# Kernel optimization log

Measured on AMD Instinct MI355X. Metric: run time of the kernel, lower is better.

## Reference

```python
import jax, jax.numpy as jnp
import numpy as np

B, C, H, W = 16, 128, 64, 64
C_OUT = 256
N_BANDS = 4
KS = [3, 5, 7, 11]
BN_EPS = 1e-5


def setup_inputs() -> dict:
    key = jax.random.key(0)
    ks = jax.random.split(key, 16)
    inp = {
        'x': jax.random.normal(ks[0], (B, C, H, W), dtype=jnp.float32),
        'conv_w0': jax.random.normal(ks[1], (C, 1, 3), dtype=jnp.float32) * 0.2,
        'conv_w1': jax.random.normal(ks[2], (C, 1, 5), dtype=jnp.float32) * 0.2,
        'conv_w2': jax.random.normal(ks[3], (C, 1, 7), dtype=jnp.float32) * 0.2,
        'conv_w3': jax.random.normal(ks[4], (C, 1, 11), dtype=jnp.float32) * 0.2,
        'bn_gamma': jax.random.uniform(ks[5], (N_BANDS, C), dtype=jnp.float32, minval=0.5, maxval=1.5),
        'bn_beta': jax.random.normal(ks[6], (N_BANDS, C), dtype=jnp.float32) * 0.1,
        'bn_mean': jax.random.normal(ks[7], (N_BANDS, C), dtype=jnp.float32) * 0.1,
        'bn_var': jax.random.uniform(ks[8], (N_BANDS, C), dtype=jnp.float32, minval=0.5, maxval=1.5),
        'scale_weights': jnp.ones((N_BANDS,), dtype=jnp.float32),
        'alpha': jnp.float32(0.5),
        'proj_w': jax.random.normal(ks[9], (C_OUT, C * N_BANDS), dtype=jnp.float32) * 0.04,
        'proj_b': jax.random.normal(ks[10], (C_OUT,), dtype=jnp.float32) * 0.02,
    }
    return inp


def _dwconv1d(xc, w):
    # xc: [B, C, L], w: [C, 1, k] depthwise, 'same' padding for odd k
    k = w.shape[-1]
    return jax.lax.conv_general_dilated(
        xc, w, window_strides=(1,), padding=[(k // 2, k // 2)],
        feature_group_count=xc.shape[1], dimension_numbers=('NCH', 'OIH', 'NCH'))


def _forward(x, conv_w0, conv_w1, conv_w2, conv_w3, bn_gamma, bn_beta, bn_mean,
             bn_var, scale_weights, alpha, proj_w, proj_b):
    b, c, h, w = x.shape
    L = h * w
    xs = x.reshape(b, c, L)                      # [B, C, L] (== x.view.transpose.transpose)
    norm_w = jax.nn.softmax(scale_weights)       # [n_bands]

    # --- multi-scale depthwise conv branch: conv -> BN(eval) -> GELU -> scale ---
    conv_bands = []
    for i, cw in enumerate([conv_w0, conv_w1, conv_w2, conv_w3]):
        y = _dwconv1d(xs, cw)                    # [B, C, L]
        inv = jax.lax.rsqrt(bn_var[i] + BN_EPS)  # [C]
        y = (y - bn_mean[i][:, None]) * (inv * bn_gamma[i])[:, None] + bn_beta[i][:, None]
        y = jax.nn.gelu(y, approximate=False)    # exact erf GELU (torch default)
        conv_bands.append(y.transpose(0, 2, 1) * norm_w[i])  # [B, L, C]

    # --- frequency band branch (interpolate to size L is identity: conv keeps L) ---
    xt = xs.transpose(0, 2, 1)                   # [B, L, C]
    Xf = jnp.fft.rfft(xt, axis=1)                # [B, n_freqs, C]
    n_freqs = L // 2 + 1
    band_size = n_freqs // N_BANDS
    fidx = jnp.arange(n_freqs)
    alpha_s = jax.nn.sigmoid(alpha)
    fused = []
    for i in range(N_BANDS):
        start = i * band_size
        end = (i + 1) * band_size if i < N_BANDS - 1 else n_freqs
        mask = (fidx >= start) & (fidx < end)
        band = jnp.fft.irfft(jnp.where(mask[None, :, None], Xf, 0), n=L, axis=1)
        fused.append(alpha_s * conv_bands[i] + (1.0 - alpha_s) * band)

    cat = jnp.concatenate(fused, axis=-1)        # [B, L, n_bands*C]
    out = cat @ proj_w.T + proj_b                # [B, L, C_out]
    return out.transpose(0, 2, 1).reshape(b, -1, h, w)


def reference(x, conv_w0, conv_w1, conv_w2, conv_w3, bn_gamma, bn_beta, bn_mean,
              bn_var, scale_weights, alpha, proj_w, proj_b):
    return _forward(x, conv_w0, conv_w1, conv_w2, conv_w3, bn_gamma, bn_beta,
                    bn_mean, bn_var, scale_weights, alpha, proj_w, proj_b)
```

## Files before the change

### kernel.cpp

```cpp
#include <hip/hip_runtime.h>
#include <math.h>

constexpr int LEN = 4096;
constexpr int NTHREADS = 512;
constexpr int PELEM = LEN / NTHREADS;
constexpr float INVN = 1.0f / 4096.0f;
constexpr float RHALF = 0.70710678118654752440f;

typedef __attribute__((ext_vector_type(8))) short bf16x8;
typedef __attribute__((ext_vector_type(4))) float f32x4;

#define APHYS(I) ((I) + ((I) >> 5))
#define TPHYS(I) ((I) + ((I) >> 5))
#define ZOFF 8

__device__ __forceinline__ unsigned short f2bf(float f) {
    unsigned u = __float_as_uint(f);
    unsigned r = (u + 0x7fffu + ((u >> 16) & 1u)) >> 16;
    return (unsigned short)r;
}

__device__ __forceinline__ int digitrev8(int j) {
    return ((j & 7) << 9) | (((j >> 3) & 7) << 6) | (((j >> 6) & 7) << 3) | (j >> 9);
}

__device__ __forceinline__ void cmul(float ar, float ai, float br, float bi,
                                     float& cr, float& ci) {
    cr = ar * br - ai * bi;
    ci = ar * bi + ai * br;
}

__device__ void dif_fft8(float* __restrict__ ar, float* __restrict__ ai,
                         const float* __restrict__ twr, const float* __restrict__ twi,
                         int tid) {
#pragma unroll
    for (int s = 0; s < 4; ++s) {
        __syncthreads();
        const int eshift = 3 * (3 - s);
        const int E = 1 << eshift;
        int j = tid & (E - 1);
        int g = tid >> eshift;
        int base = (g << (eshift + 3)) + j;

        float xr[8], xi[8];
#pragma unroll
        for (int m = 0; m < 8; ++m) {
            int idx = APHYS(base + (m << eshift));
            xr[m] = ar[idx]; xi[m] = ai[idx];
        }
        float b0r = xr[0] + xr[4], b0i = xi[0] + xi[4];
        float b1r = xr[1] + xr[5], b1i = xi[1] + xi[5];
        float b2r = xr[2] + xr[6], b2i = xi[2] + xi[6];
        float b3r = xr[3] + xr[7], b3i = xi[3] + xi[7];
        float c0r = xr[0] - xr[4], c0i = xi[0] - xi[4];
        float c1r = xr[1] - xr[5], c1i = xi[1] - xi[5];
        float c2r = xr[2] - xr[6], c2i = xi[2] - xi[6];
        float c3r = xr[3] - xr[7], c3i = xi[3] - xi[7];
        float d1r = RHALF * (c1r + c1i), d1i = RHALF * (c1i - c1r);
        float d2r = c2i,               d2i = -c2r;
        float d3r = -RHALF * (c3r - c3i), d3i = -RHALF * (c3r + c3i);
        float t0r = b0r + b2r, t0i = b0i + b2i;
        float t1r = b0r - b2r, t1i = b0i - b2i;
        float t2r = b1r + b3r, t2i = b1i + b3i;
        float t3r = b1r - b3r, t3i = b1i - b3i;
        xr[0] = t0r + t2r; xi[0] = t0i + t2i;
        xr[2] = t1r + t3i; xi[2] = t1i - t3r;
        xr[4] = t0r - t2r; xi[4] = t0i - t2i;
        xr[6] = t1r - t3i; xi[6] = t1i + t3r;
        t0r = c0r + d2r; t0i = c0i + d2i;
        t1r = c0r - d2r; t1i = c0i - d2i;
        t2r = d1r + d3r; t2i = d1i + d3i;
        t3r = d1r - d3r; t3i = d1i - d3i;
        xr[1] = t0r + t2r; xi[1] = t0i + t2i;
        xr[3] = t1r + t3i; xi[3] = t1i - t3r;
        xr[5] = t0r - t2r; xi[5] = t0i - t2i;
        xr[7] = t1r - t3i; xi[7] = t1i + t3r;

        if (s < 3) {
            int k1 = j << (3 * s);
            float w1r = twr[TPHYS(k1)], w1i = twi[TPHYS(k1)];
            float w2r, w2i, w3r, w3i, w4r, w4i, w5r, w5i, w6r, w6i, w7r, w7i;
            cmul(w1r, w1i, w1r, w1i, w2r, w2i);
            cmul(w2r, w2i, w1r, w1i, w3r, w3i);
            cmul(w2r, w2i, w2r, w2i, w4r, w4i);
            cmul(w4r, w4i, w1r, w1i, w5r, w5i);
            cmul(w4r, w4i, w2r, w2i, w6r, w6i);
            cmul(w4r, w4i, w3r, w3i, w7r, w7i);
            float orr, oii;
            cmul(xr[1], xi[1], w1r, w1i, orr, oii); xr[1] = orr; xi[1] = oii;
            cmul(xr[2], xi[2], w2r, w2i, orr, oii); xr[2] = orr; xi[2] = oii;
            cmul(xr[3], xi[3], w3r, w3i, orr, oii); xr[3] = orr; xi[3] = oii;
            cmul(xr[4], xi[4], w4r, w4i, orr, oii); xr[4] = orr; xi[4] = oii;
            cmul(xr[5], xi[5], w5r, w5i, orr, oii); xr[5] = orr; xi[5] = oii;
            cmul(xr[6], xi[6], w6r, w6i, orr, oii); xr[6] = orr; xi[6] = oii;
            cmul(xr[7], xi[7], w7r, w7i, orr, oii); xr[7] = orr; xi[7] = oii;
        }
#pragma unroll
        for (int m = 0; m < 8; ++m) {
            int idx = APHYS(base + (m << eshift));
            ar[idx] = xr[m]; ai[idx] = xi[m];
        }
    }
    __syncthreads();
}

__device__ void dit_ifft8(float* __restrict__ ar, float* __restrict__ ai,
                          const float* __restrict__ twr, const float* __restrict__ twi,
                          int tid) {
#pragma unroll
    for (int s = 0; s < 4; ++s) {
        __syncthreads();
        const int eshift = 3 * s;
        const int E = 1 << eshift;
        int j = tid & (E - 1);
        int g = tid >> eshift;
        int base = (g << (eshift + 3)) + j;

        float xr[8], xi[8];
#pragma unroll
        for (int m = 0; m < 8; ++m) {
            int idx = APHYS(base + (m << eshift));
            xr[m] = ar[idx]; xi[m] = ai[idx];
        }
        if (s > 0) {
            int k1 = j << (3 * (3 - s));
            float w1r = twr[TPHYS(k1)], w1i = -twi[TPHYS(k1)];
            float w2r, w2i, w3r, w3i, w4r, w4i, w5r, w5i, w6r, w6i, w7r, w7i;
            cmul(w1r, w1i, w1r, w1i, w2r, w2i);
            cmul(w2r, w2i, w1r, w1i, w3r, w3i);
            cmul(w2r, w2i, w2r, w2i, w4r, w4i);
            cmul(w4r, w4i, w1r, w1i, w5r, w5i);
            cmul(w4r, w4i, w2r, w2i, w6r, w6i);
            cmul(w4r, w4i, w3r, w3i, w7r, w7i);
            float orr, oii;
            cmul(xr[1], xi[1], w1r, w1i, orr, oii); xr[1] = orr; xi[1] = oii;
            cmul(xr[2], xi[2], w2r, w2i, orr, oii); xr[2] = orr; xi[2] = oii;
            cmul(xr[3], xi[3], w3r, w3i, orr, oii); xr[3] = orr; xi[3] = oii;
            cmul(xr[4], xi[4], w4r, w4i, orr, oii); xr[4] = orr; xi[4] = oii;
            cmul(xr[5], xi[5], w5r, w5i, orr, oii); xr[5] = orr; xi[5] = oii;
            cmul(xr[6], xi[6], w6r, w6i, orr, oii); xr[6] = orr; xi[6] = oii;
            cmul(xr[7], xi[7], w7r, w7i, orr, oii); xr[7] = orr; xi[7] = oii;
        }
        float b0r = xr[0] + xr[4], b0i = xi[0] + xi[4];
        float b1r = xr[1] + xr[5], b1i = xi[1] + xi[5];
        float b2r = xr[2] + xr[6], b2i = xi[2] + xi[6];
        float b3r = xr[3] + xr[7], b3i = xi[3] + xi[7];
        float c0r = xr[0] - xr[4], c0i = xi[0] - xi[4];
        float c1r = xr[1] - xr[5], c1i = xi[1] - xi[5];
        float c2r = xr[2] - xr[6], c2i = xi[2] - xi[6];
        float c3r = xr[3] - xr[7], c3i = xi[3] - xi[7];
        float d1r = RHALF * (c1r - c1i), d1i = RHALF * (c1r + c1i);
        float d2r = -c2i,              d2i = c2r;
        float d3r = -RHALF * (c3r + c3i), d3i = RHALF * (c3r - c3i);
        float t0r = b0r + b2r, t0i = b0i + b2i;
        float t1r = b0r - b2r, t1i = b0i - b2i;
        float t2r = b1r + b3r, t2i = b1i + b3i;
        float t3r = b1r - b3r, t3i = b1i - b3i;
        xr[0] = t0r + t2r; xi[0] = t0i + t2i;
        xr[2] = t1r - t3i; xi[2] = t1i + t3r;
        xr[4] = t0r - t2r; xi[4] = t0i - t2i;
        xr[6] = t1r + t3i; xi[6] = t1i - t3r;
        t0r = c0r + d2r; t0i = c0i + d2i;
        t1r = c0r - d2r; t1i = c0i - d2i;
        t2r = d1r + d3r; t2i = d1i + d3i;
        t3r = d1r - d3r; t3i = d1i - d3i;
        xr[1] = t0r + t2r; xi[1] = t0i + t2i;
        xr[3] = t1r - t3i; xi[3] = t1i + t3r;
        xr[5] = t0r - t2r; xi[5] = t0i - t2i;
        xr[7] = t1r + t3i; xi[7] = t1i - t3r;

#pragma unroll
        for (int m = 0; m < 8; ++m) {
            int idx = APHYS(base + (m << eshift));
            ar[idx] = xr[m]; ai[idx] = xi[m];
        }
    }
    __syncthreads();
}

__global__ __launch_bounds__(512) void k_bands(
    const float* __restrict__ x,
    const float* __restrict__ cw0, const float* __restrict__ cw1,
    const float* __restrict__ cw2, const float* __restrict__ cw3,
    const float* __restrict__ bng, const float* __restrict__ bnb,
    const float* __restrict__ bnm, const float* __restrict__ bnv,
    const float* __restrict__ sw, const float* __restrict__ alp,
    unsigned int* __restrict__ Fu) {
    __shared__ float zr[LEN + 16], zi[LEN + 16];
    __shared__ float wr[4224], wi[4224];
    __shared__ float twr[528], twi[528];

    const int tid = threadIdx.x;
    const int pair = blockIdx.x;
    const int b = blockIdx.y;
    const int c0 = 2 * pair, c1 = c0 + 1;

    const float* xp0 = x + ((size_t)b * 128 + c0) * LEN;
    const float* xp1 = xp0 + LEN;
#pragma unroll
    for (int p = 0; p < PELEM; ++p) {
        int l = tid + NTHREADS * p;
        float a0 = xp0[l], a1 = xp1[l];
        zr[ZOFF + l] = a0; zi[ZOFF + l] = a1;
        wr[APHYS(l)] = a0; wi[APHYS(l)] = a1;
    }
    if (tid < 8) {
        zr[tid] = 0.f; zi[tid] = 0.f;
        zr[ZOFF + LEN + tid] = 0.f; zi[ZOFF + LEN + tid] = 0.f;
    }
    {
        int jj = tid;
        float ang = -(float)(2.0 * M_PI / 4096.0) * (float)jj;
        float sv, cv;
        sincosf(ang, &sv, &cv);
        twr[TPHYS(jj)] = cv; twi[TPHYS(jj)] = sv;
    }
    dif_fft8(wr, wi, twr, twi, tid);

    float Zre[PELEM], Zim[PELEM];
#pragma unroll
    for (int p = 0; p < PELEM; ++p) {
        int l = tid + NTHREADS * p;
        Zre[p] = wr[APHYS(l)]; Zim[p] = wi[APHYS(l)];
    }

    float s0w = sw[0], s1w = sw[1], s2w = sw[2], s3w = sw[3];
    float mx = fmaxf(fmaxf(s0w, s1w), fmaxf(s2w, s3w));
    float e0 = expf(s0w - mx), e1 = expf(s1w - mx), e2 = expf(s2w - mx), e3 = expf(s3w - mx);
    float esum = e0 + e1 + e2 + e3;
    float nwv[4] = {e0 / esum, e1 / esum, e2 / esum, e3 / esum};
    float alpha_s = 1.0f / (1.0f + expf(-alp[0]));
    float oma = 1.0f - alpha_s;

    const float* cwp[4] = {cw0, cw1, cw2, cw3};
    const int kk4[4] = {3, 5, 7, 11};

    float accr[PELEM], acci[PELEM];
#pragma unroll
    for (int p = 0; p < PELEM; ++p) { accr[p] = 0.f; acci[p] = 0.f; }

    unsigned int* dst = Fu + (size_t)b * (512 * LEN / 2);
    const int n = tid & 15;

#pragma unroll
    for (int band = 0; band < 4; ++band) {
        if (band < 3) {
            const int fs = band * 512, fe = fs + 512;
#pragma unroll
            for (int p = 0; p < PELEM; ++p) {
                int j = tid + NTHREADS * p;
                int f = digitrev8(j);
                int fi = (f <= 2048) ? f : (4096 - f);
                bool keep = (fi >= fs) && (fi < fe);
                wr[APHYS(j)] = keep ? Zre[p] : 0.0f;
                wi[APHYS(j)] = keep ? Zim[p] : 0.0f;
            }
            dit_ifft8(wr, wi, twr, twi, tid);
        }

        const float* cw = cwp[band];
        const int kk = kk4[band];
        const int kh = kk >> 1;
        float w0c[11], w1c[11];
        for (int q = 0; q < kk; ++q) {
            w0c[q] = cw[c0 * kk + q];
            w1c[q] = cw[c1 * kk + q];
        }
        float A0 = rsqrtf(bnv[band * 128 + c0] + 1e-5f) * bng[band * 128 + c0];
        float B0 = bnb[band * 128 + c0] - bnm[band * 128 + c0] * A0;
        float A1 = rsqrtf(bnv[band * 128 + c1] + 1e-5f) * bng[band * 128 + c1];
        float B1 = bnb[band * 128 + c1] - bnm[band * 128 + c1] * A1;
        float nww = nwv[band];
#pragma unroll
        for (int p = 0; p < PELEM; ++p) {
            int l = tid + NTHREADS * p;
            float bvr, bvi;
            if (band < 3) {
                bvr = wr[APHYS(l)] * INVN;
                bvi = wi[APHYS(l)] * INVN;
                accr[p] += bvr;
                acci[p] += bvi;
            } else {
                bvr = zr[ZOFF + l] - accr[p];
                bvi = zi[ZOFF + l] - acci[p];
            }
            float s0 = 0.f, s1 = 0.f;
#pragma unroll
            for (int q = 0; q < 11; ++q) {
                if (q < kk) {
                    int idx = ZOFF + l + q - kh;
                    s0 += zr[idx] * w0c[q];
                    s1 += zi[idx] * w1c[q];
                }
            }
            float y0 = s0 * A0 + B0;
            y0 = 0.5f * y0 * (1.0f + erff(y0 * RHALF)) * nww;
            float y1 = s1 * A1 + B1;
            y1 = 0.5f * y1 * (1.0f + erff(y1 * RHALF)) * nww;
            float f0 = alpha_s * y0 + oma * bvr;
            float f1 = alpha_s * y1 + oma * bvi;
            int lb = (tid >> 4) + 32 * p;
            unsigned int val = (unsigned int)f2bf(f0) | ((unsigned int)f2bf(f1) << 16);
            dst[((lb * 64 + pair) * 16 + n) * 4 + band] = val;
        }
    }
}

__global__ void k_prep(const float* __restrict__ pw, unsigned short* __restrict__ Wq) {
    int idx = blockIdx.x * 256 + threadIdx.x;
    int o = idx >> 9, c = idx & 511;
    int band = c >> 7, pair = (c & 127) >> 1, lo = c & 1;
    int dstidx = (((o >> 4) * 64 + pair) * 16 + (o & 15)) * 8 + 2 * band + lo;
    Wq[dstidx] = f2bf(pw[idx]);
}

__global__ __launch_bounds__(256) void k_gemm(
    const unsigned short* __restrict__ Wq, const unsigned short* __restrict__ Fq,
    const float* __restrict__ pb, float* __restrict__ out) {
    const int tid = threadIdx.x;
    const int wave = tid >> 6, lane = tid & 63;
    const int h = lane >> 4, n16 = lane & 15;
    const int lt = blockIdx.x, b = blockIdx.y;
    const unsigned short* Fb = Fq + (size_t)b * 2097152;

    f32x4 acc[4][4];
#pragma unroll
    for (int mi = 0; mi < 4; ++mi)
#pragma unroll
        for (int ni = 0; ni < 4; ++ni) acc[mi][ni] = (f32x4){0.f, 0.f, 0.f, 0.f};

#pragma unroll
    for (int ks = 0; ks < 16; ++ks) {
        bf16x8 af[4], bfr[4];
#pragma unroll
        for (int mi = 0; mi < 4; ++mi) {
            int mb = wave * 4 + mi;
            af[mi] = *(const bf16x8*)(Wq + ((((mb * 64) + 4 * ks + h) * 16 + n16) << 3));
        }
#pragma unroll
        for (int ni = 0; ni < 4; ++ni) {
            int lb = lt * 4 + ni;
            bfr[ni] = *(const bf16x8*)(Fb + ((((lb * 64) + 4 * ks + h) * 16 + n16) << 3));
        }
#pragma unroll
        for (int mi = 0; mi < 4; ++mi)
#pragma unroll
            for (int ni = 0; ni < 4; ++ni)
                acc[mi][ni] = __builtin_amdgcn_mfma_f32_16x16x32_bf16(
                    af[mi], bfr[ni], acc[mi][ni], 0, 0, 0);
    }

#pragma unroll
    for (int mi = 0; mi < 4; ++mi) {
#pragma unroll
        for (int r = 0; r < 4; ++r) {
            int o = wave * 64 + mi * 16 + h * 4 + r;
            float bias = pb[o];
#pragma unroll
            for (int ni = 0; ni < 4; ++ni) {
                int l = lt * 64 + ni * 16 + n16;
                out[((size_t)(b * 256 + o)) * LEN + l] = acc[mi][ni][r] + bias;
            }
        }
    }
}

extern "C" void kernel_launch(void* const* d_in, const int* in_sizes, int n_in,
                              void* d_out, int out_size, void* d_ws, size_t ws_size,
                              hipStream_t stream) {
    const float* x   = (const float*)d_in[0];
    const float* cw0 = (const float*)d_in[1];
    const float* cw1 = (const float*)d_in[2];
    const float* cw2 = (const float*)d_in[3];
    const float* cw3 = (const float*)d_in[4];
    const float* bng = (const float*)d_in[5];
    const float* bnb = (const float*)d_in[6];
    const float* bnm = (const float*)d_in[7];
    const float* bnv = (const float*)d_in[8];
    const float* sw  = (const float*)d_in[9];
    const float* alp = (const float*)d_in[10];
    const float* pw  = (const float*)d_in[11];
    const float* pb  = (const float*)d_in[12];
    float* out = (float*)d_out;

    unsigned short* Wq = (unsigned short*)d_ws;
    unsigned int* Fu = (unsigned int*)((char*)d_ws + 262144);

    k_prep<<<512, 256, 0, stream>>>(pw, Wq);

    const size_t perB = (size_t)512 * LEN * 2;
    int chunk = (int)((ws_size > 262144 ? ws_size - 262144 : 0) / perB);
    if (chunk < 1) chunk = 1;
    if (chunk > 16) chunk = 16;

    for (int b0 = 0; b0 < 16; b0 += chunk) {
        int nb = 16 - b0 < chunk ? 16 - b0 : chunk;
        dim3 g1(64, nb);
        k_bands<<<g1, NTHREADS, 0, stream>>>(
            x + (size_t)b0 * 128 * LEN, cw0, cw1, cw2, cw3,
            bng, bnb, bnm, bnv, sw, alp, Fu);
        dim3 g2(64, nb);
        k_gemm<<<g2, 256, 0, stream>>>(
            Wq, (const unsigned short*)Fu, pb, out + (size_t)b0 * 256 * LEN);
    }
}
```

Baseline: 142.3 us.

## Shrink LDS footprint: bf16-packed conv input, half twiddle table, reload x from global

The fp32 zr/zi shared copies of the input are replaced by one packed bf16 pair array. The twiddle table is halved to 256 entries, and the upper half is rebuilt by rotating with a constant eighth-root factor. The residual band now reads x again from global memory instead of shared memory. Together these cut shared-memory use per block, likely so more blocks fit per CU. The cost is bf16 rounding of the conv inputs, extra bounds checks and twiddle arithmetic, and extra global reads.

```diff
diff --git a/kernel.cpp b/kernel.cpp
--- a/kernel.cpp
+++ b/kernel.cpp
@@ -6,13 +6,14 @@
 constexpr int PELEM = LEN / NTHREADS;
 constexpr float INVN = 1.0f / 4096.0f;
 constexpr float RHALF = 0.70710678118654752440f;
+constexpr float C8 = 0.92387953251128675613f;
+constexpr float S8 = -0.38268343236508977173f;
 
 typedef __attribute__((ext_vector_type(8))) short bf16x8;
 typedef __attribute__((ext_vector_type(4))) float f32x4;
 
 #define APHYS(I) ((I) + ((I) >> 5))
 #define TPHYS(I) ((I) + ((I) >> 5))
-#define ZOFF 8
 
 __device__ __forceinline__ unsigned short f2bf(float f) {
     unsigned u = __float_as_uint(f);
@@ -28,6 +29,21 @@
                                      float& cr, float& ci) {
     cr = ar * br - ai * bi;
     ci = ar * bi + ai * br;
+}
+
+template <bool CONJ>
+__device__ __forceinline__ void loadw1(const float* __restrict__ twr,
+                                       const float* __restrict__ twi, int k1,
+                                       float& w1r, float& w1i) {
+    int m = k1 & 255;
+    float c = twr[TPHYS(m)], s = twi[TPHYS(m)];
+    bool hi = (k1 & 256) != 0;
+    float cr = c * C8 - s * S8;
+    float ci = c * S8 + s * C8;
+    c = hi ? cr : c;
+    s = hi ? ci : s;
+    w1r = c;
+    w1i = CONJ ? -s : s;
 }
 
 __device__ void dif_fft8(float* __restrict__ ar, float* __restrict__ ai,
@@ -78,7 +94,8 @@
 
         if (s < 3) {
             int k1 = j << (3 * s);
-            float w1r = twr[TPHYS(k1)], w1i = twi[TPHYS(k1)];
+            float w1r, w1i;
+            loadw1<false>(twr, twi, k1, w1r, w1i);
             float w2r, w2i, w3r, w3i, w4r, w4i, w5r, w5i, w6r, w6i, w7r, w7i;
             cmul(w1r, w1i, w1r, w1i, w2r, w2i);
             cmul(w2r, w2i, w1r, w1i, w3r, w3i);
@@ -124,7 +141,8 @@
         }
         if (s > 0) {
             int k1 = j << (3 * (3 - s));
-            float w1r = twr[TPHYS(k1)], w1i = -twi[TPHYS(k1)];
+            float w1r, w1i;
+            loadw1<true>(twr, twi, k1, w1r, w1i);
             float w2r, w2i, w3r, w3i, w4r, w4i, w5r, w5i, w6r, w6i, w7r, w7i;
             cmul(w1r, w1i, w1r, w1i, w2r, w2i);
             cmul(w2r, w2i, w1r, w1i, w3r, w3i);
@@ -186,9 +204,9 @@
     const float* __restrict__ bnm, const float* __restrict__ bnv,
     const float* __restrict__ sw, const float* __restrict__ alp,
     unsigned int* __restrict__ Fu) {
-    __shared__ float zr[LEN + 16], zi[LEN + 16];
     __shared__ float wr[4224], wi[4224];
-    __shared__ float twr[528], twi[528];
+    __shared__ float twr[264], twi[264];
+    __shared__ unsigned zpk[LEN];
 
     const int tid = threadIdx.x;
     const int pair = blockIdx.x;
@@ -201,14 +219,10 @@
     for (int p = 0; p < PELEM; ++p) {
         int l = tid + NTHREADS * p;
         float a0 = xp0[l], a1 = xp1[l];
-        zr[ZOFF + l] = a0; zi[ZOFF + l] = a1;
+        zpk[l] = (unsigned)f2bf(a0) | ((unsigned)f2bf(a1) << 16);
         wr[APHYS(l)] = a0; wi[APHYS(l)] = a1;
     }
-    if (tid < 8) {
-        zr[tid] = 0.f; zi[tid] = 0.f;
-        zr[ZOFF + LEN + tid] = 0.f; zi[ZOFF + LEN + tid] = 0.f;
-    }
-    {
+    if (tid < 256) {
         int jj = tid;
         float ang = -(float)(2.0 * M_PI / 4096.0) * (float)jj;
         float sv, cv;
@@ -281,16 +295,21 @@
                 accr[p] += bvr;
                 acci[p] += bvi;
             } else {
-                bvr = zr[ZOFF + l] - accr[p];
-                bvi = zi[ZOFF + l] - acci[p];
+                bvr = xp0[l] - accr[p];
+                bvi = xp1[l] - acci[p];
             }
             float s0 = 0.f, s1 = 0.f;
 #pragma unroll
             for (int q = 0; q < 11; ++q) {
                 if (q < kk) {
-                    int idx = ZOFF + l + q - kh;
-                    s0 += zr[idx] * w0c[q];
-                    s1 += zi[idx] * w1c[q];
+                    int idx = l + q - kh;
+                    bool ok = (idx >= 0) && (idx < LEN);
+                    int ic = ok ? idx : 0;
+                    unsigned uv = zpk[ic];
+                    float v0 = ok ? __uint_as_float(uv << 16) : 0.0f;
+                    float v1 = ok ? __uint_as_float(uv & 0xffff0000u) : 0.0f;
+                    s0 += v0 * w0c[q];
+                    s1 += v1 * w1c[q];
                 }
             }
             float y0 = s0 * A0 + B0;
```

Result: slower. 147.9 us, median of 2 (+3.9%).

## Fuse last forward FFT stage, band masking and first inverse stage in registers

Applied to the files above, without the earlier changes.

The final radix-8 DIF stage is now done in registers, and the per-band frequency mask is applied straight to those outputs through a digit-reversal band lookup table. The first inverse DIT stage then runs on the same registers before anything goes to LDS. This removes one LDS write/read round trip and one barrier in the forward FFT and in each of the three inverse FFTs. The trailing __syncthreads calls in the FFT helpers were also dropped, so correctness depends on barriers elsewhere in the kernel.

```diff
diff --git a/kernel.cpp b/kernel.cpp
--- a/kernel.cpp
+++ b/kernel.cpp
@@ -20,8 +20,8 @@
     return (unsigned short)r;
 }
 
-__device__ __forceinline__ int digitrev8(int j) {
-    return ((j & 7) << 9) | (((j >> 3) & 7) << 6) | (((j >> 6) & 7) << 3) | (j >> 9);
+__device__ __forceinline__ int drev3(int t) {
+    return ((t & 7) << 6) | (((t >> 3) & 7) << 3) | (t >> 6);
 }
 
 __device__ __forceinline__ void cmul(float ar, float ai, float br, float bi,
@@ -30,152 +30,141 @@
     ci = ar * bi + ai * br;
 }
 
-__device__ void dif_fft8(float* __restrict__ ar, float* __restrict__ ai,
+__device__ __forceinline__ void dft8_fwd(float (&xr)[8], float (&xi)[8]) {
+    float b0r = xr[0] + xr[4], b0i = xi[0] + xi[4];
+    float b1r = xr[1] + xr[5], b1i = xi[1] + xi[5];
+    float b2r = xr[2] + xr[6], b2i = xi[2] + xi[6];
+    float b3r = xr[3] + xr[7], b3i = xi[3] + xi[7];
+    float c0r = xr[0] - xr[4], c0i = xi[0] - xi[4];
+    float c1r = xr[1] - xr[5], c1i = xi[1] - xi[5];
+    float c2r = xr[2] - xr[6], c2i = xi[2] - xi[6];
+    float c3r = xr[3] - xr[7], c3i = xi[3] - xi[7];
+    float d1r = RHALF * (c1r + c1i), d1i = RHALF * (c1i - c1r);
+    float d2r = c2i,               d2i = -c2r;
+    float d3r = -RHALF * (c3r - c3i), d3i = -RHALF * (c3r + c3i);
+    float t0r = b0r + b2r, t0i = b0i + b2i;
+    float t1r = b0r - b2r, t1i = b0i - b2i;
+    float t2r = b1r + b3r, t2i = b1i + b3i;
+    float t3r = b1r - b3r, t3i = b1i - b3i;
+    xr[0] = t0r + t2r; xi[0] = t0i + t2i;
+    xr[2] = t1r + t3i; xi[2] = t1i - t3r;
+    xr[4] = t0r - t2r; xi[4] = t0i - t2i;
+    xr[6] = t1r - t3i; xi[6] = t1i + t3r;
+    t0r = c0r + d2r; t0i = c0i + d2i;
+    t1r = c0r - d2r; t1i = c0i - d2i;
+    t2r = d1r + d3r; t2i = d1i + d3i;
+    t3r = d1r - d3r; t3i = d1i - d3i;
+    xr[1] = t0r + t2r; xi[1] = t0i + t2i;
+    xr[3] = t1r + t3i; xi[3] = t1i - t3r;
+    xr[5] = t0r - t2r; xi[5] = t0i - t2i;
+    xr[7] = t1r - t3i; xi[7] = t1i + t3r;
+}
+
+__device__ __forceinline__ void dft8_inv(float (&xr)[8], float (&xi)[8]) {
+    float b0r = xr[0] + xr[4], b0i = xi[0] + xi[4];
+    float b1r = xr[1] + xr[5], b1i = xi[1] + xi[5];
+    float b2r = xr[2] + xr[6], b2i = xi[2] + xi[6];
+    float b3r = xr[3] + xr[7], b3i = xi[3] + xi[7];
+    float c0r = xr[0] - xr[4], c0i = xi[0] - xi[4];
+    float c1r = xr[1] - xr[5], c1i = xi[1] - xi[5];
+    float c2r = xr[2] - xr[6], c2i = xi[2] - xi[6];
+    float c3r = xr[3] - xr[7], c3i = xi[3] - xi[7];
+    float d1r = RHALF * (c1r - c1i), d1i = RHALF * (c1r + c1i);
+    float d2r = -c2i,              d2i = c2r;
+    float d3r = -RHALF * (c3r + c3i), d3i = RHALF * (c3r - c3i);
+    float t0r = b0r + b2r, t0i = b0i + b2i;
+    float t1r = b0r - b2r, t1i = b0i - b2i;
+    float t2r = b1r + b3r, t2i = b1i + b3i;
+    float t3r = b1r - b3r, t3i = b1i - b3i;
+    xr[0] = t0r + t2r; xi[0] = t0i + t2i;
+    xr[2] = t1r - t3i; xi[2] = t1i + t3r;
+    xr[4] = t0r - t2r; xi[4] = t0i - t2i;
+    xr[6] = t1r + t3i; xi[6] = t1i - t3r;
+    t0r = c0r + d2r; t0i = c0i + d2i;
+    t1r = c0r - d2r; t1i = c0i - d2i;
+    t2r = d1r + d3r; t2i = d1i + d3i;
+    t3r = d1r - d3r; t3i = d1i - d3i;
+    xr[1] = t0r + t2r; xi[1] = t0i + t2i;
+    xr[3] = t1r - t3i; xi[3] = t1i + t3r;
+    xr[5] = t0r - t2r; xi[5] = t0i - t2i;
+    xr[7] = t1r + t3i; xi[7] = t1i - t3r;
+}
+
+template <bool CONJ>
+__device__ __forceinline__ void twmul7(float (&xr)[8], float (&xi)[8],
+                                       const float* __restrict__ twr,
+                                       const float* __restrict__ twi, int k1) {
+    float w1r = twr[TPHYS(k1)];
+    float w1i = CONJ ? -twi[TPHYS(k1)] : twi[TPHYS(k1)];
+    float w2r, w2i, w3r, w3i, w4r, w4i, w5r, w5i, w6r, w6i, w7r, w7i;
+    cmul(w1r, w1i, w1r, w1i, w2r, w2i);
+    cmul(w2r, w2i, w1r, w1i, w3r, w3i);
+    cmul(w2r, w2i, w2r, w2i, w4r, w4i);
+    cmul(w4r, w4i, w1r, w1i, w5r, w5i);
+    cmul(w4r, w4i, w2r, w2i, w6r, w6i);
+    cmul(w4r, w4i, w3r, w3i, w7r, w7i);
+    float orr, oii;
+    cmul(xr[1], xi[1], w1r, w1i, orr, oii); xr[1] = orr; xi[1] = oii;
+    cmul(xr[2], xi[2], w2r, w2i, orr, oii); xr[2] = orr; xi[2] = oii;
+    cmul(xr[3], xi[3], w3r, w3i, orr, oii); xr[3] = orr; xi[3] = oii;
+    cmul(xr[4], xi[4], w4r, w4i, orr, oii); xr[4] = orr; xi[4] = oii;
+    cmul(xr[5], xi[5], w5r, w5i, orr, oii); xr[5] = orr; xi[5] = oii;
+    cmul(xr[6], xi[6], w6r, w6i, orr, oii); xr[6] = orr; xi[6] = oii;
+    cmul(xr[7], xi[7], w7r, w7i, orr, oii); xr[7] = orr; xi[7] = oii;
+}
+
+__device__ void dif_head(float* __restrict__ ar, float* __restrict__ ai,
                          const float* __restrict__ twr, const float* __restrict__ twi,
                          int tid) {
 #pragma unroll
-    for (int s = 0; s < 4; ++s) {
+    for (int s = 0; s < 3; ++s) {
         __syncthreads();
         const int eshift = 3 * (3 - s);
         const int E = 1 << eshift;
         int j = tid & (E - 1);
         int g = tid >> eshift;
         int base = (g << (eshift + 3)) + j;
-
         float xr[8], xi[8];
 #pragma unroll
         for (int m = 0; m < 8; ++m) {
             int idx = APHYS(base + (m << eshift));
             xr[m] = ar[idx]; xi[m] = ai[idx];
         }
-        float b0r = xr[0] + xr[4], b0i = xi[0] + xi[4];
-        float b1r = xr[1] + xr[5], b1i = xi[1] + xi[5];
-        float b2r = xr[2] + xr[6], b2i = xi[2] + xi[6];
-        float b3r = xr[3] + xr[7], b3i = xi[3] + xi[7];
-        float c0r = xr[0] - xr[4], c0i = xi[0] - xi[4];
-        float c1r = xr[1] - xr[5], c1i = xi[1] - xi[5];
-        float c2r = xr[2] - xr[6], c2i = xi[2] - xi[6];
-        float c3r = xr[3] - xr[7], c3i = xi[3] - xi[7];
-        float d1r = RHALF * (c1r + c1i), d1i = RHALF * (c1i - c1r);
-        float d2r = c2i,               d2i = -c2r;
-        float d3r = -RHALF * (c3r - c3i), d3i = -RHALF * (c3r + c3i);
-        float t0r = b0r + b2r, t0i = b0i + b2i;
-        float t1r = b0r - b2r, t1i = b0i - b2i;
-        float t2r = b1r + b3r, t2i = b1i + b3i;
-        float t3r = b1r - b3r, t3i = b1i - b3i;
-        xr[0] = t0r + t2r; xi[0] = t0i + t2i;
-        xr[2] = t1r + t3i; xi[2] = t1i - t3r;
-        xr[4] = t0r - t2r; xi[4] = t0i - t2i;
-        xr[6] = t1r - t3i; xi[6] = t1i + t3r;
-        t0r = c0r + d2r; t0i = c0i + d2i;
-        t1r = c0r - d2r; t1i = c0i - d2i;
-        t2r = d1r + d3r; t2i = d1i + d3i;
-        t3r = d1r - d3r; t3i = d1i - d3i;
-        xr[1] = t0r + t2r; xi[1] = t0i + t2i;
-        xr[3] = t1r + t3i; xi[3] = t1i - t3r;
-        xr[5] = t0r - t2r; xi[5] = t0i - t2i;
-        xr[7] = t1r - t3i; xi[7] = t1i + t3r;
-
-        if (s < 3) {
-            int k1 = j << (3 * s);
-            float w1r = twr[TPHYS(k1)], w1i = twi[TPHYS(k1)];
-            float w2r, w2i, w3r, w3i, w4r, w4i, w5r, w5i, w6r, w6i, w7r, w7i;
-            cmul(w1r, w1i, w1r, w1i, w2r, w2i);
-            cmul(w2r, w2i, w1r, w1i, w3r, w3i);
-            cmul(w2r, w2i, w2r, w2i, w4r, w4i);
-            cmul(w4r, w4i, w1r, w1i, w5r, w5i);
-            cmul(w4r, w4i, w2r, w2i, w6r, w6i);
-            cmul(w4r, w4i, w3r, w3i, w7r, w7i);
-            float orr, oii;
-            cmul(xr[1], xi[1], w1r, w1i, orr, oii); xr[1] = orr; xi[1] = oii;
-            cmul(xr[2], xi[2], w2r, w2i, orr, oii); xr[2] = orr; xi[2] = oii;
-            cmul(xr[3], xi[3], w3r, w3i, orr, oii); xr[3] = orr; xi[3] = oii;
-            cmul(xr[4], xi[4], w4r, w4i, orr, oii); xr[4] = orr; xi[4] = oii;
-            cmul(xr[5], xi[5], w5r, w5i, orr, oii); xr[5] = orr; xi[5] = oii;
-            cmul(xr[6], xi[6], w6r, w6i, orr, oii); xr[6] = orr; xi[6] = oii;
-            cmul(xr[7], xi[7], w7r, w7i, orr, oii); xr[7] = orr; xi[7] = oii;
-        }
+        dft8_fwd(xr, xi);
+        twmul7<false>(xr, xi, twr, twi, j << (3 * s));
 #pragma unroll
         for (int m = 0; m < 8; ++m) {
             int idx = APHYS(base + (m << eshift));
             ar[idx] = xr[m]; ai[idx] = xi[m];
         }
     }
-    __syncthreads();
-}
-
-__device__ void dit_ifft8(float* __restrict__ ar, float* __restrict__ ai,
-                          const float* __restrict__ twr, const float* __restrict__ twi,
-                          int tid) {
-#pragma unroll
-    for (int s = 0; s < 4; ++s) {
+}
+
+__device__ void dit_tail(float* __restrict__ ar, float* __restrict__ ai,
+                         const float* __restrict__ twr, const float* __restrict__ twi,
+                         int tid) {
+#pragma unroll
+    for (int s = 1; s < 4; ++s) {
         __syncthreads();
         const int eshift = 3 * s;
         const int E = 1 << eshift;
         int j = tid & (E - 1);
         int g = tid >> eshift;
         int base = (g << (eshift + 3)) + j;
-
         float xr[8], xi[8];
 #pragma unroll
         for (int m = 0; m < 8; ++m) {
             int idx = APHYS(base + (m << eshift));
             xr[m] = ar[idx]; xi[m] = ai[idx];
         }
-        if (s > 0) {
-            int k1 = j << (3 * (3 - s));
-            float w1r = twr[TPHYS(k1)], w1i = -twi[TPHYS(k1)];
-            float w2r, w2i, w3r, w3i, w4r, w4i, w5r, w5i, w6r, w6i, w7r, w7i;
-            cmul(w1r, w1i, w1r, w1i, w2r, w2i);
-            cmul(w2r, w2i, w1r, w1i, w3r, w3i);
-            cmul(w2r, w2i, w2r, w2i, w4r, w4i);
-            cmul(w4r, w4i, w1r, w1i, w5r, w5i);
-            cmul(w4r, w4i, w2r, w2i, w6r, w6i);
-            cmul(w4r, w4i, w3r, w3i, w7r, w7i);
-            float orr, oii;
-            cmul(xr[1], xi[1], w1r, w1i, orr, oii); xr[1] = orr; xi[1] = oii;
-            cmul(xr[2], xi[2], w2r, w2i, orr, oii); xr[2] = orr; xi[2] = oii;
-            cmul(xr[3], xi[3], w3r, w3i, orr, oii); xr[3] = orr; xi[3] = oii;
-            cmul(xr[4], xi[4], w4r, w4i, orr, oii); xr[4] = orr; xi[4] = oii;
-            cmul(xr[5], xi[5], w5r, w5i, orr, oii); xr[5] = orr; xi[5] = oii;
-            cmul(xr[6], xi[6], w6r, w6i, orr, oii); xr[6] = orr; xi[6] = oii;
-            cmul(xr[7], xi[7], w7r, w7i, orr, oii); xr[7] = orr; xi[7] = oii;
-        }
-        float b0r = xr[0] + xr[4], b0i = xi[0] + xi[4];
-        float b1r = xr[1] + xr[5], b1i = xi[1] + xi[5];
-        float b2r = xr[2] + xr[6], b2i = xi[2] + xi[6];
-        float b3r = xr[3] + xr[7], b3i = xi[3] + xi[7];
-        float c0r = xr[0] - xr[4], c0i = xi[0] - xi[4];
-        float c1r = xr[1] - xr[5], c1i = xi[1] - xi[5];
-        float c2r = xr[2] - xr[6], c2i = xi[2] - xi[6];
-        float c3r = xr[3] - xr[7], c3i = xi[3] - xi[7];
-        float d1r = RHALF * (c1r - c1i), d1i = RHALF * (c1r + c1i);
-        float d2r = -c2i,              d2i = c2r;
-        float d3r = -RHALF * (c3r + c3i), d3i = RHALF * (c3r - c3i);
-        float t0r = b0r + b2r, t0i = b0i + b2i;
-        float t1r = b0r - b2r, t1i = b0i - b2i;
-        float t2r = b1r + b3r, t2i = b1i + b3i;
-        float t3r = b1r - b3r, t3i = b1i - b3i;
-        xr[0] = t0r + t2r; xi[0] = t0i + t2i;
-        xr[2] = t1r - t3i; xi[2] = t1i + t3r;
-        xr[4] = t0r - t2r; xi[4] = t0i - t2i;
-        xr[6] = t1r + t3i; xi[6] = t1i - t3r;
-        t0r = c0r + d2r; t0i = c0i + d2i;
-        t1r = c0r - d2r; t1i = c0i - d2i;
-        t2r = d1r + d3r; t2i = d1i + d3i;
-        t3r = d1r - d3r; t3i = d1i - d3i;
-        xr[1] = t0r + t2r; xi[1] = t0i + t2i;
-        xr[3] = t1r - t3i; xi[3] = t1i + t3r;
-        xr[5] = t0r - t2r; xi[5] = t0i - t2i;
-        xr[7] = t1r + t3i; xi[7] = t1i - t3r;
-
+        twmul7<true>(xr, xi, twr, twi, j << (3 * (3 - s)));
+        dft8_inv(xr, xi);
 #pragma unroll
         for (int m = 0; m < 8; ++m) {
             int idx = APHYS(base + (m << eshift));
             ar[idx] = xr[m]; ai[idx] = xi[m];
         }
     }
-    __syncthreads();
 }
 
 __global__ __launch_bounds__(512) void k_bands(
@@ -215,14 +204,20 @@
         sincosf(ang, &sv, &cv);
         twr[TPHYS(jj)] = cv; twi[TPHYS(jj)] = sv;
     }
-    dif_fft8(wr, wi, twr, twi, tid);
-
-    float Zre[PELEM], Zim[PELEM];
-#pragma unroll
-    for (int p = 0; p < PELEM; ++p) {
-        int l = tid + NTHREADS * p;
-        Zre[p] = wr[APHYS(l)]; Zim[p] = wi[APHYS(l)];
-    }
+
+    dif_head(wr, wi, twr, twi, tid);
+    float Zr[8], Zi[8];
+    __syncthreads();
+#pragma unroll
+    for (int m = 0; m < 8; ++m) {
+        int idx = APHYS(8 * tid + m);
+        Zr[m] = wr[idx]; Zi[m] = wi[idx];
+    }
+    dft8_fwd(Zr, Zi);
+
+    const int D = drev3(tid);
+    const int BM[8]  = {0, 1, 2, 3, 3, 2, 1, 0};
+    const int BM0[8] = {0, 1, 2, 3, 3, 3, 2, 1};
 
     float s0w = sw[0], s1w = sw[1], s2w = sw[2], s3w = sw[3];
     float mx = fmaxf(fmaxf(s0w, s1w), fmaxf(s2w, s3w));
@@ -245,17 +240,22 @@
 #pragma unroll
     for (int band = 0; band < 4; ++band) {
         if (band < 3) {
-            const int fs = band * 512, fe = fs + 512;
-#pragma unroll
-            for (int p = 0; p < PELEM; ++p) {
-                int j = tid + NTHREADS * p;
-                int f = digitrev8(j);
-                int fi = (f <= 2048) ? f : (4096 - f);
-                bool keep = (fi >= fs) && (fi < fe);
-                wr[APHYS(j)] = keep ? Zre[p] : 0.0f;
-                wi[APHYS(j)] = keep ? Zim[p] : 0.0f;
+            float xr[8], xi[8];
+#pragma unroll
+            for (int m = 0; m < 8; ++m) {
+                int bb = (D != 0) ? BM[m] : BM0[m];
+                bool keep = (bb == band);
+                xr[m] = keep ? Zr[m] : 0.0f;
+                xi[m] = keep ? Zi[m] : 0.0f;
             }
-            dit_ifft8(wr, wi, twr, twi, tid);
+            dft8_inv(xr, xi);
+            __syncthreads();
+#pragma unroll
+            for (int m = 0; m < 8; ++m) {
+                int idx = APHYS(8 * tid + m);
+                wr[idx] = xr[m]; wi[idx] = xi[m];
+            }
+            dit_tail(wr, wi, twr, twi, tid);
         }
 
         const float* cw = cwp[band];
```

Result: faster. 135.9 us (-4.5%).
